# Performance work log

Hardware: AMD Instinct MI355X
Metric: run time of the kernel (lower is better)

## Reference

```python
import jax, jax.numpy as jnp
import numpy as np

B, S, D = 2, 4096, 768
H, W = 12, 128          # W = one-sided attention window; S % (2*W) == 0
DFF = 3072
HD = D // H
EPS = 1e-6


def band_attention(q, k, v, w):
    """Sliding-window (banded) attention, sliding_chunks-equivalent.
    q,k,v: (B, S, H, HD); q pre-scaled by 1/sqrt(HD).
    Returns context (B, S, D) and band probs (B, H, S, 2w+1)."""
    b, s, h, hd = q.shape
    n = s // w                                    # number of query blocks
    qb = q.reshape(b, n, w, h, hd)
    kp = jnp.pad(k, ((0, 0), (w, w), (0, 0), (0, 0)))   # zero-pad seq by w each side
    vp = jnp.pad(v, ((0, 0), (w, w), (0, 0), (0, 0)))
    # block i needs padded keys [i*w, i*w + 3w)  (blocks i-1, i, i+1)
    gidx = jnp.arange(n)[:, None] * w + jnp.arange(3 * w)[None, :]   # (n, 3w)
    kb = kp[:, gidx]                              # (b, n, 3w, h, hd)
    vb = vp[:, gidx]
    scores = jnp.einsum('bnthd,bnjhd->bhntj', qb, kb)   # (b,h,n,w,3w)
    t = jnp.arange(w)[:, None]                    # (w,1) pos within block
    j = jnp.arange(3 * w)[None, :]                # (1,3w)
    rel = j - w - t                               # relative key offset, valid in [-w,w]
    pos = jnp.arange(n)[:, None, None] * w + (j - w)     # (n,1,3w) global key pos
    valid = (jnp.abs(rel) <= w)[None] & (pos >= 0) & (pos < s)  # (n,w,3w)
    scores = jnp.where(valid[None, None], scores, -jnp.inf)
    probs = jax.nn.softmax(scores, axis=-1)
    out = jnp.einsum('bhntj,bnjhd->bnthd', probs, vb).reshape(b, s, h * hd)
    # extract the (2w+1) diagonals: offset d -> column j = t + d
    jj = jnp.arange(w)[:, None] + jnp.arange(2 * w + 1)[None, :]     # (w, 2w+1)
    attw = jnp.take_along_axis(probs, jj[None, None, None], axis=-1)
    return out, attw.reshape(b, h, s, 2 * w + 1)


def setup_inputs() -> dict:
    key = jax.random.key(0)
    ks = jax.random.split(key, 12)
    def lin(k, fan_in, shape):
        return (jax.random.normal(k, shape, jnp.float32) / np.sqrt(fan_in)).astype(jnp.float32)
    return {
        'src': jax.random.normal(ks[0], (B, S, D), jnp.float32),
        'Wq': lin(ks[1], D, (D, D)), 'bq': jnp.zeros((D,), jnp.float32),
        'Wk': lin(ks[2], D, (D, D)), 'bk': jnp.zeros((D,), jnp.float32),
        'Wv': lin(ks[3], D, (D, D)), 'bv': jnp.zeros((D,), jnp.float32),
        'W1': lin(ks[4], D, (D, DFF)), 'b1': jnp.zeros((DFF,), jnp.float32),
        'W2': lin(ks[5], DFF, (DFF, D)), 'b2': jnp.zeros((D,), jnp.float32),
        'g2': 1.0 + 0.1 * jax.random.normal(ks[6], (D,), jnp.float32),
        'beta2': 0.1 * jax.random.normal(ks[7], (D,), jnp.float32),
    }


def reference(src, Wq, bq, Wk, bk, Wv, bv, W1, b1, W2, b2, g2, beta2):
    b, s, d = src.shape
    # self-attention (allenai LongformerSelfAttention: q/k/v linears, no out proj)
    q = ((src @ Wq + bq) / np.sqrt(HD).astype(np.float32)).reshape(b, s, H, HD)
    k = (src @ Wk + bk).reshape(b, s, H, HD)
    v = (src @ Wv + bv).reshape(b, s, H, HD)
    attn_out, attn_w = band_attention(q, k, v, W)
    x = src + attn_out                      # residual (dropout=0, eval)
    # PositionalwiseFeedForward: Linear -> ReLU -> Linear
    ffn = jnp.maximum(x @ W1 + b1, 0.0) @ W2 + b2
    y = x + ffn
    # post-norm (normalize_before=False: only norm2 is applied)
    mu = jnp.mean(y, axis=-1, keepdims=True)
    var = jnp.mean(jnp.square(y - mu), axis=-1, keepdims=True)
    out = g2 * (y - mu) / jnp.sqrt(var + EPS) + beta2
    return out, attn_w
```

## Files before the change

kernel.cpp:

```cpp
#include <hip/hip_runtime.h>
#include <hip/hip_bf16.h>
#include <stdint.h>

#define NB 2
#define NS 4096
#define ND 768
#define NH 12
#define NW 128
#define NDFF 3072
#define NHD 64
#define NCH 32

typedef __attribute__((ext_vector_type(8))) short bf16x8;
typedef __attribute__((ext_vector_type(4))) short s16x4;
typedef __attribute__((ext_vector_type(4))) float f32x4;

__device__ __forceinline__ float bf2f(short u) {
    union { unsigned int i; float f; } c;
    c.i = ((unsigned int)(unsigned short)u) << 16;
    return c.f;
}
__device__ __forceinline__ short f2bf(float f) {
    union { float f; unsigned int i; } c;
    c.f = f;
    unsigned int x = c.i;
    return (short)((x + 0x7fffu + ((x >> 16) & 1u)) >> 16);
}

__device__ __forceinline__ void gl16(const void* g, const void* l) {
    __builtin_amdgcn_global_load_lds(
        (const __attribute__((address_space(1))) void*)g,
        (__attribute__((address_space(3))) void*)l, 16, 0, 0);
}

__global__ __launch_bounds__(256) void cast_bf16(const float* __restrict__ in,
                                                 short* __restrict__ out, int n4) {
    int i = blockIdx.x * 256 + threadIdx.x;
    if (i < n4) {
        f32x4 v = ((const f32x4*)in)[i];
        s16x4 o;
        o[0] = f2bf(v[0]); o[1] = f2bf(v[1]); o[2] = f2bf(v[2]); o[3] = f2bf(v[3]);
        ((s16x4*)out)[i] = o;
    }
}

__global__ __launch_bounds__(256) void transpose_cast(const float* __restrict__ in,
                                                      short* __restrict__ out,
                                                      int K, int N) {
    __shared__ float tile[32][33];
    int kb = blockIdx.y * 32, nb = blockIdx.x * 32;
    int tx = threadIdx.x & 31, ty = threadIdx.x >> 5;
    #pragma unroll
    for (int r = ty; r < 32; r += 8)
        tile[r][tx] = in[(long)(kb + r) * N + nb + tx];
    __syncthreads();
    #pragma unroll
    for (int r = ty; r < 32; r += 8)
        out[(long)(nb + r) * K + kb + tx] = f2bf(tile[tx][r]);
}

template<int MODE>
__global__ __launch_bounds__(256, 2) void gemmdb(
    const short* __restrict__ A,
    const short* __restrict__ Bt,
    const float* __restrict__ b0,
    const float* __restrict__ b1,
    const float* __restrict__ b2,
    void* __restrict__ outp,
    const float* __restrict__ xres,
    int M, int N, int K, int gx)
{
    __shared__ short lds[2][256 * 64];
    const int KT = K >> 6;

    int cpx = gridDim.x >> 3;
    int bid = blockIdx.x;
    int tile = (bid & 7) * cpx + (bid >> 3);
    int n0 = (tile % gx) * 128;
    int m0 = (tile / gx) * 128;

    int tid = threadIdx.x;
    int wid = tid >> 6, lane = tid & 63;
    int wr = wid >> 1, wc = wid & 1;
    int g = lane >> 4, lr = lane & 15;

    int rl = lane >> 3, sl = lane & 7;
    int soff = (sl ^ rl) << 3;
    const short* gA[4];
    const short* gB[4];
    #pragma unroll
    for (int c = 0; c < 4; ++c) {
        int row = c * 32 + wid * 8 + rl;
        gA[c] = A + (long)(m0 + row) * K + soff;
        gB[c] = Bt + (long)(n0 + row) * K + soff;
    }

    f32x4 acc[4][4];
    #pragma unroll
    for (int a = 0; a < 4; ++a)
        #pragma unroll
        for (int c = 0; c < 4; ++c)
            acc[a][c] = (f32x4){0.f, 0.f, 0.f, 0.f};

    auto stage = [&](int t, int buf) {
        long ko = (long)t << 6;
        #pragma unroll
        for (int c = 0; c < 4; ++c) {
            int lbase = (c * 32 + wid * 8) * 64;
            gl16(gA[c] + ko, &lds[buf][lbase]);
            gl16(gB[c] + ko, &lds[buf][128 * 64 + lbase]);
        }
    };

    stage(0, 0);
    asm volatile("s_waitcnt vmcnt(0)" ::: "memory");
    __builtin_amdgcn_s_barrier();

    int buf = 0;
    for (int t = 0; t < KT; ++t) {
        if (t + 1 < KT) stage(t + 1, buf ^ 1);
        const short* bufA = lds[buf];
        const short* bufB = lds[buf] + 128 * 64;
        bf16x8 af[2][4], bfr[2][4];
        #pragma unroll
        for (int kk = 0; kk < 2; ++kk) {
            int ph = (((kk << 2) + g) ^ (lr & 7)) << 3;
            #pragma unroll
            for (int mt = 0; mt < 4; ++mt)
                af[kk][mt] = *(const bf16x8*)&bufA[(wr * 64 + mt * 16 + lr) * 64 + ph];
            #pragma unroll
            for (int nt = 0; nt < 4; ++nt)
                bfr[kk][nt] = *(const bf16x8*)&bufB[(wc * 64 + nt * 16 + lr) * 64 + ph];
        }
        #pragma unroll
        for (int kk = 0; kk < 2; ++kk)
            #pragma unroll
            for (int mt = 0; mt < 4; ++mt)
                #pragma unroll
                for (int nt = 0; nt < 4; ++nt)
                    acc[mt][nt] = __builtin_amdgcn_mfma_f32_16x16x32_bf16(
                        af[kk][mt], bfr[kk][nt], acc[mt][nt], 0, 0, 0);
        asm volatile("s_waitcnt vmcnt(0)" ::: "memory");
        __builtin_amdgcn_s_barrier();
        buf ^= 1;
    }

    int mr0 = m0 + wr * 64;
    int nc0 = n0 + wc * 64;
    if (MODE == 4) {
        int proj = n0 / 768;
        const float* bp = (proj == 0) ? b0 : (proj == 1) ? b1 : b2;
        float scl = (proj == 0) ? 0.125f : 1.0f;
        short* obase = (short*)outp + (long)proj * ((long)NB * NS * ND);
        #pragma unroll
        for (int mt = 0; mt < 4; ++mt) {
            #pragma unroll
            for (int nt = 0; nt < 4; ++nt) {
                int c = nc0 + nt * 16 + lr - proj * 768;
                int hh = c >> 6, hd = c & 63;
                float bv = bp[c];
                if (proj == 2) {
                    int m = mr0 + mt * 16 + (g << 2);
                    int bbi = m >> 12, s = m & (NS - 1);
                    s16x4 ov;
                    ov[0] = f2bf(acc[mt][nt][0] + bv);
                    ov[1] = f2bf(acc[mt][nt][1] + bv);
                    ov[2] = f2bf(acc[mt][nt][2] + bv);
                    ov[3] = f2bf(acc[mt][nt][3] + bv);
                    *(s16x4*)&obase[((long)(bbi * NH + hh) * NHD + hd) * NS + s] = ov;
                } else {
                    #pragma unroll
                    for (int i = 0; i < 4; ++i) {
                        int m = mr0 + mt * 16 + (g << 2) + i;
                        int bbi = m >> 12, s = m & (NS - 1);
                        obase[((long)(bbi * NH + hh) * NS + s) * NHD + hd] =
                            f2bf((acc[mt][nt][i] + bv) * scl);
                    }
                }
            }
        }
    } else {
        #pragma unroll
        for (int mt = 0; mt < 4; ++mt) {
            #pragma unroll
            for (int nt = 0; nt < 4; ++nt) {
                int col = nc0 + nt * 16 + lr;
                float bv = b0[col];
                #pragma unroll
                for (int i = 0; i < 4; ++i) {
                    int m = mr0 + mt * 16 + (g << 2) + i;
                    float v = acc[mt][nt][i];
                    if (MODE == 2) {
                        v = fmaxf(v + bv, 0.f);
                        ((short*)outp)[(long)m * NDFF + col] = f2bf(v);
                    } else {
                        v = v + bv + xres[(long)m * ND + col];
                        ((float*)outp)[(long)m * ND + col] = v;
                    }
                }
            }
        }
    }
}

#define KLD 72
#define PLD 392
#define ATT_LDS (384 * KLD * 2 + 128 * PLD * 2)

__global__ __launch_bounds__(512) void attn_kernel(
    const short* __restrict__ qg,
    const short* __restrict__ kg,
    const short* __restrict__ vtg,
    const float* __restrict__ src,
    float* __restrict__ attw,
    float* __restrict__ x,
    short* __restrict__ xb)
{
    extern __shared__ char smem[];
    short* kv = (short*)smem;
    short* pl = (short*)(smem + 384 * KLD * 2);

    int blk = blockIdx.x;
    int ch = blk & 31;
    int tmp = blk >> 5;
    int h = tmp % NH;
    int b = tmp / NH;
    int tid = threadIdx.x;
    int wid = tid >> 6;
    int lane = tid & 63;
    int g = lane >> 4, lr = lane & 15;
    long bh = (long)(b * NH + h);
    long kbase = bh * NS * NHD;
    int srow0 = ch * NW;

    #pragma unroll
    for (int it = 0; it < 6; ++it) {
        int idx = it * 512 + tid;
        int j = idx >> 3;
        int c = (idx & 7) << 3;
        int s = srow0 - NW + j;
        bf16x8 v = {};
        if (s >= 0 && s < NS)
            v = *(const bf16x8*)&kg[kbase + (long)s * NHD + c];
        *(bf16x8*)&kv[j * KLD + c] = v;
    }

    int t0 = wid << 4;
    bf16x8 aq[2];
    #pragma unroll
    for (int kk = 0; kk < 2; ++kk)
        aq[kk] = *(const bf16x8*)&qg[kbase + (long)(srow0 + t0 + lr) * NHD + (kk << 5) + (g << 3)];

    __syncthreads();

    f32x4 sc[24];
    #pragma unroll
    for (int jt = 0; jt < 24; ++jt) {
        f32x4 a = (f32x4){0.f, 0.f, 0.f, 0.f};
        #pragma unroll
        for (int kk = 0; kk < 2; ++kk) {
            bf16x8 bk = *(const bf16x8*)&kv[(jt * 16 + lr) * KLD + (kk << 5) + (g << 3)];
            a = __builtin_amdgcn_mfma_f32_16x16x32_bf16(aq[kk], bk, a, 0, 0, 0);
        }
        sc[jt] = a;
    }

    float mx[4] = {-3.0e30f, -3.0e30f, -3.0e30f, -3.0e30f};
    #pragma unroll
    for (int jt = 0; jt < 24; ++jt) {
        int j = jt * 16 + lr;
        int sp = srow0 - NW + j;
        bool pok = (sp >= 0) && (sp < NS);
        #pragma unroll
        for (int i = 0; i < 4; ++i) {
            int t = t0 + (g << 2) + i;
            bool ok = pok && (j >= t) && (j <= t + 2 * NW);
            float v = ok ? sc[jt][i] : -3.0e30f;
            sc[jt][i] = v;
            mx[i] = fmaxf(mx[i], v);
        }
    }
    #pragma unroll
    for (int m = 1; m < 16; m <<= 1) {
        #pragma unroll
        for (int i = 0; i < 4; ++i)
            mx[i] = fmaxf(mx[i], __shfl_xor(mx[i], m, 64));
    }
    float sm[4] = {0.f, 0.f, 0.f, 0.f};
    #pragma unroll
    for (int jt = 0; jt < 24; ++jt) {
        #pragma unroll
        for (int i = 0; i < 4; ++i) {
            float v = sc[jt][i];
            float p = (v > -1.0e30f) ? __expf(v - mx[i]) : 0.0f;
            sc[jt][i] = p;
            sm[i] += p;
        }
    }
    #pragma unroll
    for (int m = 1; m < 16; m <<= 1) {
        #pragma unroll
        for (int i = 0; i < 4; ++i)
            sm[i] += __shfl_xor(sm[i], m, 64);
    }
    float inv[4];
    #pragma unroll
    for (int i = 0; i < 4; ++i) inv[i] = 1.0f / sm[i];

    #pragma unroll
    for (int jt = 0; jt < 24; ++jt) {
        #pragma unroll
        for (int i = 0; i < 4; ++i)
            pl[(t0 + (g << 2) + i) * PLD + jt * 16 + lr] = f2bf(sc[jt][i] * inv[i]);
    }

    __syncthreads();

    #pragma unroll
    for (int it = 0; it < 6; ++it) {
        int idx = it * 512 + tid;
        int hd = idx / 48;
        int c = (idx % 48) << 3;
        int s0 = srow0 - NW + c;
        bf16x8 v = {};
        if (s0 >= 0 && s0 < NS)
            v = *(const bf16x8*)&vtg[(bh * NHD + hd) * NS + s0];
        *(bf16x8*)&kv[hd * PLD + c] = v;
    }
    __syncthreads();

    f32x4 o[4];
    #pragma unroll
    for (int nt = 0; nt < 4; ++nt) o[nt] = (f32x4){0.f, 0.f, 0.f, 0.f};
    #pragma unroll
    for (int kt = 0; kt < 12; ++kt) {
        bf16x8 ap = *(const bf16x8*)&pl[(t0 + lr) * PLD + (kt << 5) + (g << 3)];
        #pragma unroll
        for (int nt = 0; nt < 4; ++nt) {
            bf16x8 bv = *(const bf16x8*)&kv[(nt * 16 + lr) * PLD + (kt << 5) + (g << 3)];
            o[nt] = __builtin_amdgcn_mfma_f32_16x16x32_bf16(ap, bv, o[nt], 0, 0, 0);
        }
    }

    #pragma unroll
    for (int nt = 0; nt < 4; ++nt) {
        int d = nt * 16 + lr;
        int dcol = h * NHD + d;
        #pragma unroll
        for (int i = 0; i < 4; ++i) {
            int t = t0 + (g << 2) + i;
            long row = (long)b * NS + srow0 + t;
            float v = o[nt][i] + src[row * ND + dcol];
            x[row * ND + dcol] = v;
            xb[row * ND + dcol] = f2bf(v);
        }
    }

    long aw = (bh * NS + srow0) * 257;
    for (int t = t0; t < t0 + 16; ++t) {
        long rowbase = aw + (long)t * 257;
        int pb = t * PLD + t;
        for (int c = lane; c < 257; c += 64)
            attw[rowbase + c] = bf2f(pl[pb + c]);
    }
}

__global__ __launch_bounds__(256) void ln_kernel(float* __restrict__ y,
                                                 const float* __restrict__ g2,
                                                 const float* __restrict__ beta2) {
    int row = blockIdx.x;
    long base = (long)row * ND;
    int tid = threadIdx.x;
    float v[3];
    float s = 0.f, ss = 0.f;
    #pragma unroll
    for (int i = 0; i < 3; ++i) {
        v[i] = y[base + i * 256 + tid];
        s += v[i];
        ss += v[i] * v[i];
    }
    #pragma unroll
    for (int m = 1; m < 64; m <<= 1) {
        s += __shfl_xor(s, m, 64);
        ss += __shfl_xor(ss, m, 64);
    }
    __shared__ float red[8];
    int wid = tid >> 6, lane = tid & 63;
    if (lane == 0) { red[wid] = s; red[wid + 4] = ss; }
    __syncthreads();
    s = red[0] + red[1] + red[2] + red[3];
    ss = red[4] + red[5] + red[6] + red[7];
    float mu = s * (1.0f / ND);
    float var = ss * (1.0f / ND) - mu * mu;
    float rstd = rsqrtf(var + 1e-6f);
    #pragma unroll
    for (int i = 0; i < 3; ++i) {
        int c = i * 256 + tid;
        y[base + c] = g2[c] * (v[i] - mu) * rstd + beta2[c];
    }
}

extern "C" void kernel_launch(void* const* d_in, const int* in_sizes, int n_in,
                              void* d_out, int out_size, void* d_ws, size_t ws_size,
                              hipStream_t stream) {
    const float* src  = (const float*)d_in[0];
    const float* Wq   = (const float*)d_in[1];
    const float* bq   = (const float*)d_in[2];
    const float* Wk   = (const float*)d_in[3];
    const float* bk   = (const float*)d_in[4];
    const float* Wv   = (const float*)d_in[5];
    const float* bv   = (const float*)d_in[6];
    const float* W1   = (const float*)d_in[7];
    const float* b1   = (const float*)d_in[8];
    const float* W2   = (const float*)d_in[9];
    const float* b2   = (const float*)d_in[10];
    const float* g2   = (const float*)d_in[11];
    const float* bt2  = (const float*)d_in[12];

    float* out  = (float*)d_out;
    float* attw = out + (long)NB * NS * ND;

    char* ws = (char*)d_ws;
    const size_t SZ_XF  = (size_t)NB * NS * ND * 4;
    const size_t SZ_XB  = (size_t)NB * NS * ND * 2;
    const size_t SZ_W1T = (size_t)ND * NDFF * 2;
    const size_t SZ_W2T = (size_t)NDFF * ND * 2;
    const size_t SZ_QKV = (size_t)NB * NS * ND * 2;
    const size_t SZ_WT  = (size_t)ND * ND * 2;

    float* x_f32 = (float*)ws;
    short* x_bf  = (short*)(ws + SZ_XF);
    short* W1T   = (short*)(ws + SZ_XF + SZ_XB);
    short* W2T   = (short*)(ws + SZ_XF + SZ_XB + SZ_W1T);
    char*  regA  = ws + SZ_XF + SZ_XB + SZ_W1T + SZ_W2T;
    short* srcb  = (short*)regA;
    short* WqT   = (short*)(regA + SZ_QKV);
    short* WkT   = (short*)(regA + SZ_QKV + SZ_WT);
    short* WvT   = (short*)(regA + SZ_QKV + 2 * SZ_WT);
    short* qb    = (short*)(regA + SZ_QKV + 3 * SZ_WT);
    short* kb_   = (short*)(regA + 2 * SZ_QKV + 3 * SZ_WT);
    short* vb_   = (short*)(regA + 3 * SZ_QKV + 3 * SZ_WT);
    short* hbuf  = (short*)regA;

    const int M = NB * NS;

    cast_bf16<<<(M * ND / 4 + 255) / 256, 256, 0, stream>>>(src, srcb, M * ND / 4);
    transpose_cast<<<dim3(ND / 32, ND / 32), 256, 0, stream>>>(Wq, WqT, ND, ND);
    transpose_cast<<<dim3(ND / 32, ND / 32), 256, 0, stream>>>(Wk, WkT, ND, ND);
    transpose_cast<<<dim3(ND / 32, ND / 32), 256, 0, stream>>>(Wv, WvT, ND, ND);
    transpose_cast<<<dim3(NDFF / 32, ND / 32), 256, 0, stream>>>(W1, W1T, ND, NDFF);
    transpose_cast<<<dim3(ND / 32, NDFF / 32), 256, 0, stream>>>(W2, W2T, NDFF, ND);

    gemmdb<4><<<(2304 / 128) * (M / 128), 256, 0, stream>>>(
        srcb, WqT, bq, bk, bv, qb, nullptr, M, 2304, ND, 2304 / 128);

    (void)hipFuncSetAttribute(reinterpret_cast<const void*>(attn_kernel),
                              hipFuncAttributeMaxDynamicSharedMemorySize, ATT_LDS);
    attn_kernel<<<NB * NH * NCH, 512, ATT_LDS, stream>>>(qb, kb_, vb_, src, attw, x_f32, x_bf);

    gemmdb<2><<<(NDFF / 128) * (M / 128), 256, 0, stream>>>(
        x_bf, W1T, b1, b1, b1, hbuf, nullptr, M, NDFF, ND, NDFF / 128);
    gemmdb<3><<<(ND / 128) * (M / 128), 256, 0, stream>>>(
        hbuf, W2T, b2, b2, b2, out, x_f32, M, ND, NDFF, ND / 128);

    ln_kernel<<<M, 256, 0, stream>>>(out, g2, bt2);
}
```

Measured before the change: 257.5 us.

## Prefetch V into registers early and write band probabilities directly from registers

The global loads of the transposed V tile are issued before the QK^T and softmax phase and held in registers, then stored to shared memory after the probabilities are written, so their latency overlaps the compute. The attention-weight output is now written straight from the fp32 softmax registers during the probability store, replacing the separate trailing loop that re-read bf16 probabilities from shared memory. This removes a shared-memory readback pass and keeps the band weights at fp32 instead of bf16-rounded values. The cost is extra register pressure from the 6 prefetched vectors, and strided, scattered global writes for attw. Explicit barriers with waitcnt replace __syncthreads.

Result: no change. 254.2 us (-1.3%).

```diff
diff --git a/kernel.cpp b/kernel.cpp
--- a/kernel.cpp
+++ b/kernel.cpp
@@ -245,77 +245,7 @@
         *(bf16x8*)&kv[j * KLD + c] = v;
     }
 
-    int t0 = wid << 4;
-    bf16x8 aq[2];
-    #pragma unroll
-    for (int kk = 0; kk < 2; ++kk)
-        aq[kk] = *(const bf16x8*)&qg[kbase + (long)(srow0 + t0 + lr) * NHD + (kk << 5) + (g << 3)];
-
-    __syncthreads();
-
-    f32x4 sc[24];
-    #pragma unroll
-    for (int jt = 0; jt < 24; ++jt) {
-        f32x4 a = (f32x4){0.f, 0.f, 0.f, 0.f};
-        #pragma unroll
-        for (int kk = 0; kk < 2; ++kk) {
-            bf16x8 bk = *(const bf16x8*)&kv[(jt * 16 + lr) * KLD + (kk << 5) + (g << 3)];
-            a = __builtin_amdgcn_mfma_f32_16x16x32_bf16(aq[kk], bk, a, 0, 0, 0);
-        }
-        sc[jt] = a;
-    }
-
-    float mx[4] = {-3.0e30f, -3.0e30f, -3.0e30f, -3.0e30f};
-    #pragma unroll
-    for (int jt = 0; jt < 24; ++jt) {
-        int j = jt * 16 + lr;
-        int sp = srow0 - NW + j;
-        bool pok = (sp >= 0) && (sp < NS);
-        #pragma unroll
-        for (int i = 0; i < 4; ++i) {
-            int t = t0 + (g << 2) + i;
-            bool ok = pok && (j >= t) && (j <= t + 2 * NW);
-            float v = ok ? sc[jt][i] : -3.0e30f;
-            sc[jt][i] = v;
-            mx[i] = fmaxf(mx[i], v);
-        }
-    }
-    #pragma unroll
-    for (int m = 1; m < 16; m <<= 1) {
-        #pragma unroll
-        for (int i = 0; i < 4; ++i)
-            mx[i] = fmaxf(mx[i], __shfl_xor(mx[i], m, 64));
-    }
-    float sm[4] = {0.f, 0.f, 0.f, 0.f};
-    #pragma unroll
-    for (int jt = 0; jt < 24; ++jt) {
-        #pragma unroll
-        for (int i = 0; i < 4; ++i) {
-            float v = sc[jt][i];
-            float p = (v > -1.0e30f) ? __expf(v - mx[i]) : 0.0f;
-            sc[jt][i] = p;
-            sm[i] += p;
-        }
-    }
-    #pragma unroll
-    for (int m = 1; m < 16; m <<= 1) {
-        #pragma unroll
-        for (int i = 0; i < 4; ++i)
-            sm[i] += __shfl_xor(sm[i], m, 64);
-    }
-    float inv[4];
-    #pragma unroll
-    for (int i = 0; i < 4; ++i) inv[i] = 1.0f / sm[i];
-
-    #pragma unroll
-    for (int jt = 0; jt < 24; ++jt) {
-        #pragma unroll
-        for (int i = 0; i < 4; ++i)
-            pl[(t0 + (g << 2) + i) * PLD + jt * 16 + lr] = f2bf(sc[jt][i] * inv[i]);
-    }
-
-    __syncthreads();
-
+    bf16x8 vreg[6];
     #pragma unroll
     for (int it = 0; it < 6; ++it) {
         int idx = it * 512 + tid;
@@ -325,9 +255,101 @@
         bf16x8 v = {};
         if (s0 >= 0 && s0 < NS)
             v = *(const bf16x8*)&vtg[(bh * NHD + hd) * NS + s0];
-        *(bf16x8*)&kv[hd * PLD + c] = v;
-    }
+        vreg[it] = v;
+    }
+
+    int t0 = wid << 4;
+    bf16x8 aq[2];
+    #pragma unroll
+    for (int kk = 0; kk < 2; ++kk)
+        aq[kk] = *(const bf16x8*)&qg[kbase + (long)(srow0 + t0 + lr) * NHD + (kk << 5) + (g << 3)];
+
     __syncthreads();
+
+    f32x4 sc[24];
+    #pragma unroll
+    for (int jt = 0; jt < 24; ++jt) {
+        f32x4 a = (f32x4){0.f, 0.f, 0.f, 0.f};
+        #pragma unroll
+        for (int kk = 0; kk < 2; ++kk) {
+            bf16x8 bk = *(const bf16x8*)&kv[(jt * 16 + lr) * KLD + (kk << 5) + (g << 3)];
+            a = __builtin_amdgcn_mfma_f32_16x16x32_bf16(aq[kk], bk, a, 0, 0, 0);
+        }
+        sc[jt] = a;
+    }
+
+    float mx[4] = {-3.0e30f, -3.0e30f, -3.0e30f, -3.0e30f};
+    #pragma unroll
+    for (int jt = 0; jt < 24; ++jt) {
+        int j = jt * 16 + lr;
+        int sp = srow0 - NW + j;
+        bool pok = (sp >= 0) && (sp < NS);
+        #pragma unroll
+        for (int i = 0; i < 4; ++i) {
+            int t = t0 + (g << 2) + i;
+            bool ok = pok && (j >= t) && (j <= t + 2 * NW);
+            float v = ok ? sc[jt][i] : -3.0e30f;
+            sc[jt][i] = v;
+            mx[i] = fmaxf(mx[i], v);
+        }
+    }
+    #pragma unroll
+    for (int m = 1; m < 16; m <<= 1) {
+        #pragma unroll
+        for (int i = 0; i < 4; ++i)
+            mx[i] = fmaxf(mx[i], __shfl_xor(mx[i], m, 64));
+    }
+    float sm[4] = {0.f, 0.f, 0.f, 0.f};
+    #pragma unroll
+    for (int jt = 0; jt < 24; ++jt) {
+        #pragma unroll
+        for (int i = 0; i < 4; ++i) {
+            float v = sc[jt][i];
+            float p = (v > -1.0e30f) ? __expf(v - mx[i]) : 0.0f;
+            sc[jt][i] = p;
+            sm[i] += p;
+        }
+    }
+    #pragma unroll
+    for (int m = 1; m < 16; m <<= 1) {
+        #pragma unroll
+        for (int i = 0; i < 4; ++i)
+            sm[i] += __shfl_xor(sm[i], m, 64);
+    }
+    float inv[4];
+    #pragma unroll
+    for (int i = 0; i < 4; ++i) inv[i] = 1.0f / sm[i];
+
+    long aw = (bh * NS + srow0) * 257;
+    #pragma unroll
+    for (int jt = 0; jt < 24; ++jt) {
+        int j = jt * 16 + lr;
+        #pragma unroll
+        for (int i = 0; i < 4; ++i) {
+            int t = t0 + (g << 2) + i;
+            float pv = sc[jt][i] * inv[i];
+            pl[t * PLD + j] = f2bf(pv);
+            int c = j - t;
+            if (c >= 0 && c <= 2 * NW)
+                attw[aw + (long)t * 257 + c] = pv;
+        }
+    }
+
+    asm volatile("s_waitcnt lgkmcnt(0)" ::: "memory");
+    __builtin_amdgcn_s_barrier();
+    __builtin_amdgcn_sched_barrier(0);
+
+    #pragma unroll
+    for (int it = 0; it < 6; ++it) {
+        int idx = it * 512 + tid;
+        int hd = idx / 48;
+        int c = (idx % 48) << 3;
+        *(bf16x8*)&kv[hd * PLD + c] = vreg[it];
+    }
+
+    asm volatile("s_waitcnt lgkmcnt(0)" ::: "memory");
+    __builtin_amdgcn_s_barrier();
+    __builtin_amdgcn_sched_barrier(0);
 
     f32x4 o[4];
     #pragma unroll
@@ -354,14 +376,6 @@
             x[row * ND + dcol] = v;
             xb[row * ND + dcol] = f2bf(v);
         }
-    }
-
-    long aw = (bh * NS + srow0) * 257;
-    for (int t = t0; t < t0 + 16; ++t) {
-        long rowbase = aw + (long)t * 257;
-        int pb = t * PLD + t;
-        for (int c = lane; c < 257; c += 64)
-            attw[rowbase + c] = bf2f(pl[pb + c]);
     }
 }
 
```
